# Kernel tuning notes

Measured on AMD Instinct MI355X. Metric: run time of the kernel, lower is better.

The kernel has to match this reference:

```python
import jax, jax.numpy as jnp
import numpy as np

N, NFEAT, NHID, NCLASS, E = 100000, 128, 128, 40, 1600000

def _glorot(key, fan_in, fan_out):
    lim = float(np.sqrt(6.0 / (fan_in + fan_out)))
    return jax.random.uniform(key, (fan_in, fan_out), jnp.float32, -lim, lim)

def setup_inputs() -> dict:
    key = jax.random.key(0)
    ks = jax.random.split(key, 20)
    inp = {
        'x': jax.random.normal(ks[0], (N, NFEAT), jnp.float32),
        'edge_index': jax.random.randint(ks[1], (2, E), 0, N, jnp.int64 if jax.config.x64_enabled else jnp.int32),
    }
    dims = [(NFEAT, NHID), (NHID, NHID), (NHID, NHID), (NHID, NHID), (NHID, NHID), (NHID, NHID)]
    names = ['gc1_w1', 'gc1_w2', 'gc2_w1', 'gc2_w2', 'gc3_w1', 'gc3_w2']
    for i, (nm, (fi, fo)) in enumerate(zip(names, dims)):
        inp[nm] = _glorot(ks[2 + i], fi, fo)
        inp[nm.replace('w', 'b')] = jnp.zeros((fo,), jnp.float32)
    inp['lin1_w'] = _glorot(ks[10], 3 * NHID, 3 * NHID)
    inp['lin1_b'] = jnp.zeros((3 * NHID,), jnp.float32)
    inp['lin2_w'] = _glorot(ks[11], 3 * NHID, NCLASS)
    inp['lin2_b'] = jnp.zeros((NCLASS,), jnp.float32)
    return inp

def _gin_conv(x, src, dst, w1, b1, w2, b2):
    # GINConv, eps=0: mlp(x + sum_{j->i} x_j)
    agg = jax.ops.segment_sum(x[src], dst, num_segments=N)  # [N, d]
    h = jax.nn.relu((x + agg) @ w1 + b1)
    return jax.nn.relu(h @ w2 + b2)

def reference(x, edge_index, gc1_w1, gc1_b1, gc1_w2, gc1_b2,
              gc2_w1, gc2_b1, gc2_w2, gc2_b2,
              gc3_w1, gc3_b1, gc3_w2, gc3_b2,
              lin1_w, lin1_b, lin2_w, lin2_b):
    src, dst = edge_index[0], edge_index[1]
    h1 = _gin_conv(x, src, dst, gc1_w1, gc1_b1, gc1_w2, gc1_b2)
    h2 = _gin_conv(h1, src, dst, gc2_w1, gc2_b1, gc2_w2, gc2_b2)
    h3 = _gin_conv(h2, src, dst, gc3_w1, gc3_b1, gc3_w2, gc3_b2)
    h = jnp.concatenate([h1, h2, h3], axis=1)  # [N, 3*nhid]
    h = jax.nn.relu(h @ lin1_w + lin1_b)  # dropout inactive in eval mode
    h = h @ lin2_w + lin2_b
    return jax.nn.log_softmax(h, axis=1)
```

## Files before the change

### kernel.cpp

```cpp
#include <hip/hip_runtime.h>

#define N_NODES 100000
#define NEDGE   1600000
#define NHID    128
#define NCLASS  40

#define AGG_NODES 128
#define COLV_LDS  3072
#define FILL_SLICES 8
#define FILL_RANGE  12500

using bf16x8 = __attribute__((ext_vector_type(8))) short;
using f32x4  = __attribute__((ext_vector_type(4))) float;

__device__ __forceinline__ float bf2f(unsigned short s) {
    unsigned u = ((unsigned)s) << 16; float f; __builtin_memcpy(&f, &u, 4); return f;
}
__device__ __forceinline__ unsigned short f2bf(float f) {
    unsigned u; __builtin_memcpy(&u, &f, 4);
    u = u + 0x7fffu + ((u >> 16) & 1u);
    return (unsigned short)(u >> 16);
}

__device__ __forceinline__ void gld16(const void* g, void* l) {
    __builtin_amdgcn_global_load_lds(g, l, 16, 0, 0);
}

__global__ void k_zero(int* __restrict__ p, int n) {
    int i = blockIdx.x * 256 + threadIdx.x;
    if (i < n) p[i] = 0;
}

__global__ void k_count(const int* __restrict__ ei, int* __restrict__ cnt) {
    int e = blockIdx.x * 256 + threadIdx.x;
    if (e < NEDGE) atomicAdd(&cnt[ei[NEDGE + e]], 1);
}

__global__ void k_scan1(const int* __restrict__ cnt, int* __restrict__ rp, int* __restrict__ bsum) {
    __shared__ int sh[256];
    int t = threadIdx.x, base = blockIdx.x * 1024;
    int v[4]; int s = 0;
    for (int k = 0; k < 4; ++k) { int i = base + t * 4 + k; v[k] = (i < N_NODES) ? cnt[i] : 0; s += v[k]; }
    sh[t] = s; __syncthreads();
    for (int off = 1; off < 256; off <<= 1) {
        int x = (t >= off) ? sh[t - off] : 0;
        __syncthreads();
        sh[t] += x;
        __syncthreads();
    }
    int excl = sh[t] - s;
    for (int k = 0; k < 4; ++k) { int i = base + t * 4 + k; if (i < N_NODES) rp[i] = excl; excl += v[k]; }
    if (t == 255) bsum[blockIdx.x] = sh[255];
}

__global__ void k_scan2(int* __restrict__ bsum, int nb) {
    __shared__ int sh[256];
    int t = threadIdx.x;
    int v = (t < nb) ? bsum[t] : 0;
    sh[t] = v; __syncthreads();
    for (int off = 1; off < 256; off <<= 1) {
        int x = (t >= off) ? sh[t - off] : 0;
        __syncthreads();
        sh[t] += x;
        __syncthreads();
    }
    if (t < nb) bsum[t] = sh[t] - v;
}

__global__ void k_scan3(int* __restrict__ rp, const int* __restrict__ bsum) {
    int base = blockIdx.x * 1024;
    int off = bsum[blockIdx.x];
    for (int k = 0; k < 4; ++k) {
        int i = base + threadIdx.x * 4 + k;
        if (i < N_NODES) rp[i] += off;
    }
    if (blockIdx.x == 0 && threadIdx.x == 0) rp[N_NODES] = NEDGE;
}

__global__ __launch_bounds__(256) void k_fillr(const int* __restrict__ ei, const int* __restrict__ rp,
                                               int* __restrict__ cur, int* __restrict__ colv) {
    int slice = blockIdx.x & 7;
    int e = (blockIdx.x >> 3) * 256 + threadIdx.x;
    if (e >= NEDGE) return;
    int d = ei[NEDGE + e];
    int lo = slice * FILL_RANGE;
    if (d >= lo && d < lo + FILL_RANGE) {
        int p = atomicAdd(&cur[d], 1);
        colv[rp[d] + p] = ei[e];
    }
}

__global__ void k_wprep(const float* __restrict__ w, unsigned short* __restrict__ wt,
                        int K, int O, int Opad) {
    int idx = blockIdx.x * 256 + threadIdx.x;
    if (idx >= K * Opad) return;
    int kss = K >> 5;
    int e = idx & 7, lane = (idx >> 3) & 63, rest = idx >> 9;
    int ks = rest % kss, ot = rest / kss;
    int c = ot * 16 + (lane & 15);
    int k = ks * 32 + (lane >> 4) * 8 + e;
    float v = (c < O) ? w[k * O + c] : 0.f;
    wt[idx] = f2bf(v);
}

__global__ void k_xprep(const float* __restrict__ x, unsigned short* __restrict__ xs) {
    int s = blockIdx.x & 7;
    int rest = (blockIdx.x >> 3) * 256 + threadIdx.x;
    if (rest >= N_NODES * 8) return;
    int n = rest >> 3, wrd = rest & 7;
    float2 v = *(const float2*)(x + (size_t)n * 128 + s * 16 + wrd * 2);
    ((unsigned*)xs)[(size_t)s * N_NODES * 8 + rest] =
        (unsigned)f2bf(v.x) | ((unsigned)f2bf(v.y) << 16);
}

__device__ __forceinline__ void acc8(float* acc, uint4 f, float m) {
    unsigned u[4] = {f.x, f.y, f.z, f.w};
    for (int d = 0; d < 4; ++d) {
        acc[2 * d]     = fmaf(m, bf2f((unsigned short)u[d]), acc[2 * d]);
        acc[2 * d + 1] = fmaf(m, bf2f((unsigned short)(u[d] >> 16)), acc[2 * d + 1]);
    }
}

__global__ __launch_bounds__(256) void k_aggs(const unsigned short* __restrict__ feat,
                                              unsigned short* __restrict__ tout,
                                              const int* __restrict__ rp,
                                              const int* __restrict__ colv) {
    __shared__ int scol[COLV_LDS];
    __shared__ int srp[AGG_NODES + 1];
    const int s = blockIdx.x & 7;
    const int chunk = blockIdx.x >> 3;
    const int tid = threadIdx.x;
    const int nbase = chunk * AGG_NODES;

    for (int i = tid; i <= AGG_NODES; i += 256) {
        int n = nbase + i;
        srp[i] = rp[n <= N_NODES ? n : N_NODES];
    }
    __syncthreads();
    const int ebase = srp[0];
    const int ecount = srp[AGG_NODES] - ebase;
    const int elds = ecount < COLV_LDS ? ecount : COLV_LDS;
    for (int i = tid; i < elds; i += 256) scol[i] = colv[ebase + i];
    __syncthreads();

    const unsigned* fs = (const unsigned*)feat + (size_t)s * N_NODES * 8;
    unsigned* ts = (unsigned*)tout + (size_t)s * N_NODES * 8;

    const int sub = tid >> 1, half = tid & 1;
    const int node = nbase + sub;
    if (node >= N_NODES) return;
    const int off = half * 4;
    const int e0 = srp[sub] - ebase, e1 = srp[sub + 1] - ebase;

    float acc[8];
    {
        uint4 a = *(const uint4*)(fs + (size_t)node * 8 + off);
        unsigned u[4] = {a.x, a.y, a.z, a.w};
        for (int d = 0; d < 4; ++d) {
            acc[2 * d]     = bf2f((unsigned short)u[d]);
            acc[2 * d + 1] = bf2f((unsigned short)(u[d] >> 16));
        }
    }

    for (int e = e0; e < e1; e += 8) {
        int j[8]; float m[8];
        #pragma unroll
        for (int k = 0; k < 8; ++k) {
            int ee = e + k;
            bool v = ee < e1;
            int idx = ee < COLV_LDS ? scol[ee] : colv[ebase + ee];
            j[k] = v ? idx : node;
            m[k] = v ? 1.f : 0.f;
        }
        uint4 f[8];
        #pragma unroll
        for (int k = 0; k < 8; ++k)
            f[k] = *(const uint4*)(fs + (size_t)j[k] * 8 + off);
        #pragma unroll
        for (int k = 0; k < 8; ++k) acc8(acc, f[k], m[k]);
    }

    uint4 o;
    o.x = (unsigned)f2bf(acc[0]) | ((unsigned)f2bf(acc[1]) << 16);
    o.y = (unsigned)f2bf(acc[2]) | ((unsigned)f2bf(acc[3]) << 16);
    o.z = (unsigned)f2bf(acc[4]) | ((unsigned)f2bf(acc[5]) << 16);
    o.w = (unsigned)f2bf(acc[6]) | ((unsigned)f2bf(acc[7]) << 16);
    *(uint4*)(ts + (size_t)node * 8 + off) = o;
}

__global__ __launch_bounds__(256) void k_mlp(
    const unsigned short* __restrict__ tin,
    const unsigned short* __restrict__ w1t, const float* __restrict__ b1,
    const unsigned short* __restrict__ w2t, const float* __restrict__ b2,
    unsigned short* __restrict__ hout) {
    __shared__ __align__(16) char tlds[64 * 256];
    __shared__ __align__(16) char hlds[64 * 256];
    const int tid = threadIdx.x, lane = tid & 63, w = tid >> 6;
    const int l15 = lane & 15, lg = lane >> 4;
    const int nbase = blockIdx.x * 64;

    #pragma unroll
    for (int i = 0; i < 4; ++i) {
        int byte = w * 4096 + i * 1024 + lane * 16;
        int r = byte >> 8, c8s = (byte >> 4) & 15;
        int c8 = c8s ^ (r & 7);
        int slice = c8 >> 1, half = c8 & 1;
        int node = nbase + r; if (node >= N_NODES) node = 0;
        gld16(tin + ((size_t)slice * N_NODES + node) * 16 + half * 8,
              tlds + w * 4096 + i * 1024);
    }

    bf16x8 B1[2][4]; float bias1[2]; int cols[2];
    #pragma unroll
    for (int ot = 0; ot < 2; ++ot) {
        int c = (w * 2 + ot) * 16 + l15;
        cols[ot] = c; bias1[ot] = b1[c];
        #pragma unroll
        for (int ks = 0; ks < 4; ++ks)
            B1[ot][ks] = *(const bf16x8*)(w1t + ((size_t)((w * 2 + ot) * 4 + ks) * 64 + lane) * 8);
    }
    __syncthreads();

    {
        bf16x8 A[2][4];
        #pragma unroll
        for (int ks = 0; ks < 4; ++ks)
            A[0][ks] = *(const bf16x8*)(tlds + l15 * 256 + ((ks * 64 + lg * 16) ^ ((l15 & 7) << 4)));
        #pragma unroll
        for (int m = 0; m < 4; ++m) {
            int cur = m & 1, nxt = cur ^ 1;
            if (m < 3) {
                int row = (m + 1) * 16 + l15;
                #pragma unroll
                for (int ks = 0; ks < 4; ++ks)
                    A[nxt][ks] = *(const bf16x8*)(tlds + row * 256 + ((ks * 64 + lg * 16) ^ ((row & 7) << 4)));
            }
            #pragma unroll
            for (int ot = 0; ot < 2; ++ot) {
                f32x4 acc = {0.f, 0.f, 0.f, 0.f};
                #pragma unroll
                for (int ks = 0; ks < 4; ++ks)
                    acc = __builtin_amdgcn_mfma_f32_16x16x32_bf16(A[cur][ks], B1[ot][ks], acc, 0, 0, 0);
                int c2 = cols[ot] * 2;
                #pragma unroll
                for (int r = 0; r < 4; ++r) {
                    int row = m * 16 + lg * 4 + r;
                    float v = acc[r] + bias1[ot]; v = v > 0.f ? v : 0.f;
                    *(unsigned short*)(hlds + row * 256 + (c2 ^ ((row & 7) << 4))) = f2bf(v);
                }
            }
        }
    }

    bf16x8 B2[2][4]; float bias2[2];
    #pragma unroll
    for (int ot = 0; ot < 2; ++ot) {
        bias2[ot] = b2[cols[ot]];
        #pragma unroll
        for (int ks = 0; ks < 4; ++ks)
            B2[ot][ks] = *(const bf16x8*)(w2t + ((size_t)((w * 2 + ot) * 4 + ks) * 64 + lane) * 8);
    }
    __syncthreads();

    {
        bf16x8 A[2][4];
        #pragma unroll
        for (int ks = 0; ks < 4; ++ks)
            A[0][ks] = *(const bf16x8*)(hlds + l15 * 256 + ((ks * 64 + lg * 16) ^ ((l15 & 7) << 4)));
        #pragma unroll
        for (int m = 0; m < 4; ++m) {
            int cur = m & 1, nxt = cur ^ 1;
            if (m < 3) {
                int row = (m + 1) * 16 + l15;
                #pragma unroll
                for (int ks = 0; ks < 4; ++ks)
                    A[nxt][ks] = *(const bf16x8*)(hlds + row * 256 + ((ks * 64 + lg * 16) ^ ((row & 7) << 4)));
            }
            #pragma unroll
            for (int ot = 0; ot < 2; ++ot) {
                f32x4 acc = {0.f, 0.f, 0.f, 0.f};
                #pragma unroll
                for (int ks = 0; ks < 4; ++ks)
                    acc = __builtin_amdgcn_mfma_f32_16x16x32_bf16(A[cur][ks], B2[ot][ks], acc, 0, 0, 0);
                int cslice = cols[ot] >> 4, cw = cols[ot] & 15;
                #pragma unroll
                for (int r = 0; r < 4; ++r) {
                    int node = nbase + m * 16 + lg * 4 + r;
                    if (node < N_NODES) {
                        float v = acc[r] + bias2[ot]; v = v > 0.f ? v : 0.f;
                        hout[((size_t)cslice * N_NODES + node) * 16 + cw] = f2bf(v);
                    }
                }
            }
        }
    }
}

__global__ __launch_bounds__(512, 2) void k_final(
    const unsigned short* __restrict__ h1, const unsigned short* __restrict__ h2,
    const unsigned short* __restrict__ h3,
    const unsigned short* __restrict__ l1t, const float* __restrict__ l1b,
    const unsigned short* __restrict__ l2t, const float* __restrict__ l2b,
    float* __restrict__ out) {
    extern __shared__ __align__(16) char lds[];
    const int tid = threadIdx.x, lane = tid & 63, w = tid >> 6;
    const int l15 = lane & 15, lg = lane >> 4;
    const int nbase = blockIdx.x * 128;

    #pragma unroll
    for (int i = 0; i < 12; ++i) {
        unsigned byte = (unsigned)(w * 12288 + i * 1024 + lane * 16);
        unsigned r = byte / 768u;
        unsigned rem = byte - r * 768u;
        int c8 = (int)(rem >> 4) ^ (int)(r & 7);
        int part = c8 >> 4, c8p = c8 & 15;
        int slice = c8p >> 1, half = c8p & 1;
        int node = nbase + (int)r; if (node >= N_NODES) node = 0;
        const unsigned short* hp = part == 0 ? h1 : (part == 1 ? h2 : h3);
        gld16(hp + ((size_t)slice * N_NODES + node) * 16 + half * 8,
              lds + w * 12288 + i * 1024);
    }

    bf16x8 B[2][3];
    #pragma unroll
    for (int ot = 0; ot < 3; ++ot)
        B[0][ot] = *(const bf16x8*)(l1t + ((size_t)((w * 3 + ot) * 12) * 64 + lane) * 8);
    __syncthreads();

    f32x4 acc[8][3];
    #pragma unroll
    for (int m = 0; m < 8; ++m)
        #pragma unroll
        for (int ot = 0; ot < 3; ++ot) acc[m][ot] = {0.f, 0.f, 0.f, 0.f};
    {
        #pragma unroll
        for (int ks = 0; ks < 12; ++ks) {
            int cur = ks & 1, nxt = cur ^ 1;
            if (ks < 11) {
                #pragma unroll
                for (int ot = 0; ot < 3; ++ot)
                    B[nxt][ot] = *(const bf16x8*)(l1t + ((size_t)((w * 3 + ot) * 12 + ks + 1) * 64 + lane) * 8);
            }
            bf16x8 A[8];
            #pragma unroll
            for (int m = 0; m < 8; ++m) {
                int row = m * 16 + l15;
                A[m] = *(const bf16x8*)(lds + row * 768 + ((ks * 64 + lg * 16) ^ ((row & 7) << 4)));
            }
            #pragma unroll
            for (int ot = 0; ot < 3; ++ot)
                #pragma unroll
                for (int m = 0; m < 8; ++m)
                    acc[m][ot] = __builtin_amdgcn_mfma_f32_16x16x32_bf16(A[m], B[cur][ot], acc[m][ot], 0, 0, 0);
        }
    }
    __syncthreads();

    #pragma unroll
    for (int ot = 0; ot < 3; ++ot) {
        int c = (w * 3 + ot) * 16 + l15;
        float bias = l1b[c];
        #pragma unroll
        for (int m = 0; m < 8; ++m)
            #pragma unroll
            for (int r = 0; r < 4; ++r) {
                int row = m * 16 + lg * 4 + r;
                float v = acc[m][ot][r] + bias; v = v > 0.f ? v : 0.f;
                *(unsigned short*)(lds + row * 768 + ((c * 2) ^ ((row & 7) << 4))) = f2bf(v);
            }
    }
    __syncthreads();

    f32x4 acc2[3];
    #pragma unroll
    for (int ot = 0; ot < 3; ++ot) acc2[ot] = {0.f, 0.f, 0.f, 0.f};
    {
        const int row = w * 16 + l15;
        bf16x8 C2[2][3]; bf16x8 A2[2];
        #pragma unroll
        for (int ot = 0; ot < 3; ++ot)
            C2[0][ot] = *(const bf16x8*)(l2t + ((size_t)(ot * 12) * 64 + lane) * 8);
        A2[0] = *(const bf16x8*)(lds + row * 768 + ((lg * 16) ^ ((row & 7) << 4)));
        #pragma unroll
        for (int ks = 0; ks < 12; ++ks) {
            int cur = ks & 1, nxt = cur ^ 1;
            if (ks < 11) {
                #pragma unroll
                for (int ot = 0; ot < 3; ++ot)
                    C2[nxt][ot] = *(const bf16x8*)(l2t + ((size_t)(ot * 12 + ks + 1) * 64 + lane) * 8);
                A2[nxt] = *(const bf16x8*)(lds + row * 768 + (((ks + 1) * 64 + lg * 16) ^ ((row & 7) << 4)));
            }
            #pragma unroll
            for (int ot = 0; ot < 3; ++ot)
                acc2[ot] = __builtin_amdgcn_mfma_f32_16x16x32_bf16(A2[cur], C2[cur][ot], acc2[ot], 0, 0, 0);
        }
    }

    int c0 = l15;
    #pragma unroll
    for (int r = 0; r < 4; ++r) {
        float v0 = acc2[0][r] + l2b[c0];
        float v1 = acc2[1][r] + l2b[c0 + 16];
        float v2 = (c0 < 8) ? (acc2[2][r] + l2b[c0 + 32]) : -1e30f;
        float mx = fmaxf(fmaxf(v0, v1), v2);
        for (int msk = 1; msk < 16; msk <<= 1) mx = fmaxf(mx, __shfl_xor(mx, msk));
        float s = __expf(v0 - mx) + __expf(v1 - mx) + ((c0 < 8) ? __expf(v2 - mx) : 0.f);
        for (int msk = 1; msk < 16; msk <<= 1) s += __shfl_xor(s, msk);
        float lse = mx + __logf(s);
        int node = nbase + w * 16 + lg * 4 + r;
        if (node < N_NODES) {
            out[(size_t)node * 40 + c0] = v0 - lse;
            out[(size_t)node * 40 + c0 + 16] = v1 - lse;
            if (c0 < 8) out[(size_t)node * 40 + c0 + 32] = v2 - lse;
        }
    }
}

extern "C" void kernel_launch(void* const* d_in, const int* in_sizes, int n_in,
                              void* d_out, int out_size, void* d_ws, size_t ws_size,
                              hipStream_t stream) {
    const float* x  = (const float*)d_in[0];
    const int*   ei = (const int*)d_in[1];
    const float* gw1[3] = {(const float*)d_in[2],  (const float*)d_in[6],  (const float*)d_in[10]};
    const float* gb1[3] = {(const float*)d_in[3],  (const float*)d_in[7],  (const float*)d_in[11]};
    const float* gw2[3] = {(const float*)d_in[4],  (const float*)d_in[8],  (const float*)d_in[12]};
    const float* gb2[3] = {(const float*)d_in[5],  (const float*)d_in[9],  (const float*)d_in[13]};
    const float* l1w = (const float*)d_in[14];
    const float* l1b = (const float*)d_in[15];
    const float* l2w = (const float*)d_in[16];
    const float* l2b = (const float*)d_in[17];
    float* out = (float*)d_out;

    char* p = (char*)d_ws;
    auto alloc = [&](size_t bytes) { char* q = p; p += (bytes + 255) & ~(size_t)255; return q; };
    int* rp   = (int*)alloc(4 * (N_NODES + 1));
    int* cnt  = (int*)alloc(4 * N_NODES);
    int* bsum = (int*)alloc(4 * 256);
    int* colv = (int*)alloc(4 * (size_t)NEDGE);
    unsigned short* t  = (unsigned short*)alloc(2 * (size_t)N_NODES * 128);
    unsigned short* h1 = (unsigned short*)alloc(2 * (size_t)N_NODES * 128);
    unsigned short* h2 = (unsigned short*)alloc(2 * (size_t)N_NODES * 128);
    unsigned short* h3 = (unsigned short*)alloc(2 * (size_t)N_NODES * 128);
    unsigned short* xs = h3;
    unsigned short* wt[6];
    for (int i = 0; i < 6; ++i) wt[i] = (unsigned short*)alloc(2 * 128 * 128);
    unsigned short* l1t = (unsigned short*)alloc(2 * 384 * 384);
    unsigned short* l2t = (unsigned short*)alloc(2 * 48 * 384);

    static bool attr_set = false;
    if (!attr_set) {
        hipFuncSetAttribute((const void*)k_final,
                            hipFuncAttributeMaxDynamicSharedMemorySize, 128 * 768);
        attr_set = true;
    }

    const int nb = (N_NODES + 1023) / 1024;
    k_zero<<<(N_NODES + 255) / 256, 256, 0, stream>>>(cnt, N_NODES);
    k_count<<<(NEDGE + 255) / 256, 256, 0, stream>>>(ei, cnt);
    k_scan1<<<nb, 256, 0, stream>>>(cnt, rp, bsum);
    k_scan2<<<1, 256, 0, stream>>>(bsum, nb);
    k_scan3<<<nb, 256, 0, stream>>>(rp, bsum);
    k_zero<<<(N_NODES + 255) / 256, 256, 0, stream>>>(cnt, N_NODES);
    k_fillr<<<((NEDGE + 255) / 256) * FILL_SLICES, 256, 0, stream>>>(ei, rp, cnt, colv);

    for (int i = 0; i < 3; ++i) {
        k_wprep<<<(128 * 128 + 255) / 256, 256, 0, stream>>>(gw1[i], wt[2 * i], 128, 128, 128);
        k_wprep<<<(128 * 128 + 255) / 256, 256, 0, stream>>>(gw2[i], wt[2 * i + 1], 128, 128, 128);
    }
    k_wprep<<<(384 * 384 + 255) / 256, 256, 0, stream>>>(l1w, l1t, 384, 384, 384);
    k_wprep<<<(384 * 48 + 255) / 256, 256, 0, stream>>>(l2w, l2t, 384, 40, 48);

    k_xprep<<<8 * ((N_NODES * 8 + 255) / 256), 256, 0, stream>>>(x, xs);

    const int gagg = ((N_NODES + AGG_NODES - 1) / AGG_NODES) * 8;
    const int gtile = (N_NODES + 63) / 64;
    const int gtile2 = (N_NODES + 127) / 128;
    k_aggs<<<gagg, 256, 0, stream>>>(xs, t, rp, colv);
    k_mlp<<<gtile, 256, 0, stream>>>(t, wt[0], gb1[0], wt[1], gb2[0], h1);
    k_aggs<<<gagg, 256, 0, stream>>>(h1, t, rp, colv);
    k_mlp<<<gtile, 256, 0, stream>>>(t, wt[2], gb1[1], wt[3], gb2[1], h2);
    k_aggs<<<gagg, 256, 0, stream>>>(h2, t, rp, colv);
    k_mlp<<<gtile, 256, 0, stream>>>(t, wt[4], gb1[2], wt[5], gb2[2], h3);
    k_final<<<gtile2, 512, 128 * 768, stream>>>(h1, h2, h3, l1t, l1b, l2t, l2b, out);
}
```

Measured before the change: 520.6 us.

## Merge weight-prep launches, slice edge counting, and deepen weight prefetch

The eight per-matrix weight conversion launches become one kernel that indexes across all weight matrices. That kernel writes into a single destination assumed to be contiguous with the later weight buffers, which relies on the allocator placing them back to back. Edge-degree counting now partitions destinations into eight ranges, as the fill kernel already does, to localize atomics, at the cost of re-reading the edge list eight times. The MLP kernel loads its second-layer weights before the first barrier, and the final kernel prefetches B fragments two steps ahead with a triple buffer, both to hide global-load latency at the cost of more registers.

```diff
diff --git a/kernel.cpp b/kernel.cpp
--- a/kernel.cpp
+++ b/kernel.cpp
@@ -9,6 +9,7 @@
 #define COLV_LDS  3072
 #define FILL_SLICES 8
 #define FILL_RANGE  12500
+#define WPREP_TOT   264192
 
 using bf16x8 = __attribute__((ext_vector_type(8))) short;
 using f32x4  = __attribute__((ext_vector_type(4))) float;
@@ -31,9 +32,13 @@
     if (i < n) p[i] = 0;
 }
 
-__global__ void k_count(const int* __restrict__ ei, int* __restrict__ cnt) {
-    int e = blockIdx.x * 256 + threadIdx.x;
-    if (e < NEDGE) atomicAdd(&cnt[ei[NEDGE + e]], 1);
+__global__ __launch_bounds__(256) void k_countr(const int* __restrict__ ei, int* __restrict__ cnt) {
+    int slice = blockIdx.x & 7;
+    int e = (blockIdx.x >> 3) * 256 + threadIdx.x;
+    if (e >= NEDGE) return;
+    int d = ei[NEDGE + e];
+    int lo = slice * FILL_RANGE;
+    if (d >= lo && d < lo + FILL_RANGE) atomicAdd(&cnt[d], 1);
 }
 
 __global__ void k_scan1(const int* __restrict__ cnt, int* __restrict__ rp, int* __restrict__ bsum) {
@@ -90,17 +95,29 @@
     }
 }
 
-__global__ void k_wprep(const float* __restrict__ w, unsigned short* __restrict__ wt,
-                        int K, int O, int Opad) {
+__global__ void k_wprep_all(const float* __restrict__ g0, const float* __restrict__ g1,
+                            const float* __restrict__ g2, const float* __restrict__ g3,
+                            const float* __restrict__ g4, const float* __restrict__ g5,
+                            const float* __restrict__ l1w, const float* __restrict__ l2w,
+                            unsigned short* __restrict__ dst) {
     int idx = blockIdx.x * 256 + threadIdx.x;
-    if (idx >= K * Opad) return;
+    if (idx >= WPREP_TOT) return;
+    const float* w; int local, K, O;
+    if (idx < 98304) {
+        int r = idx >> 14; local = idx & 16383; K = 128; O = 128;
+        w = r == 0 ? g0 : r == 1 ? g1 : r == 2 ? g2 : r == 3 ? g3 : r == 4 ? g4 : g5;
+    } else if (idx < 245760) {
+        local = idx - 98304; K = 384; O = 384; w = l1w;
+    } else {
+        local = idx - 245760; K = 384; O = 40; w = l2w;
+    }
     int kss = K >> 5;
-    int e = idx & 7, lane = (idx >> 3) & 63, rest = idx >> 9;
+    int e = local & 7, lane = (local >> 3) & 63, rest = local >> 9;
     int ks = rest % kss, ot = rest / kss;
     int c = ot * 16 + (lane & 15);
     int k = ks * 32 + (lane >> 4) * 8 + e;
     float v = (c < O) ? w[k * O + c] : 0.f;
-    wt[idx] = f2bf(v);
+    dst[idx] = f2bf(v);
 }
 
 __global__ void k_xprep(const float* __restrict__ x, unsigned short* __restrict__ xs) {
@@ -219,6 +236,14 @@
         for (int ks = 0; ks < 4; ++ks)
             B1[ot][ks] = *(const bf16x8*)(w1t + ((size_t)((w * 2 + ot) * 4 + ks) * 64 + lane) * 8);
     }
+    bf16x8 B2[2][4]; float bias2[2];
+    #pragma unroll
+    for (int ot = 0; ot < 2; ++ot) {
+        bias2[ot] = b2[(w * 2 + ot) * 16 + l15];
+        #pragma unroll
+        for (int ks = 0; ks < 4; ++ks)
+            B2[ot][ks] = *(const bf16x8*)(w2t + ((size_t)((w * 2 + ot) * 4 + ks) * 64 + lane) * 8);
+    }
     __syncthreads();
 
     {
@@ -250,15 +275,6 @@
                 }
             }
         }
-    }
-
-    bf16x8 B2[2][4]; float bias2[2];
-    #pragma unroll
-    for (int ot = 0; ot < 2; ++ot) {
-        bias2[ot] = b2[cols[ot]];
-        #pragma unroll
-        for (int ks = 0; ks < 4; ++ks)
-            B2[ot][ks] = *(const bf16x8*)(w2t + ((size_t)((w * 2 + ot) * 4 + ks) * 64 + lane) * 8);
     }
     __syncthreads();
 
@@ -321,10 +337,12 @@
               lds + w * 12288 + i * 1024);
     }
 
-    bf16x8 B[2][3];
-    #pragma unroll
-    for (int ot = 0; ot < 3; ++ot)
-        B[0][ot] = *(const bf16x8*)(l1t + ((size_t)((w * 3 + ot) * 12) * 64 + lane) * 8);
+    bf16x8 B[3][3];
+    #pragma unroll
+    for (int ot = 0; ot < 3; ++ot) {
+        B[0][ot] = *(const bf16x8*)(l1t + ((size_t)((w * 3 + ot) * 12 + 0) * 64 + lane) * 8);
+        B[1][ot] = *(const bf16x8*)(l1t + ((size_t)((w * 3 + ot) * 12 + 1) * 64 + lane) * 8);
+    }
     __syncthreads();
 
     f32x4 acc[8][3];
@@ -335,11 +353,12 @@
     {
         #pragma unroll
         for (int ks = 0; ks < 12; ++ks) {
-            int cur = ks & 1, nxt = cur ^ 1;
-            if (ks < 11) {
+            int cur = ks % 3;
+            if (ks < 10) {
+                int nx2 = (ks + 2) % 3;
                 #pragma unroll
                 for (int ot = 0; ot < 3; ++ot)
-                    B[nxt][ot] = *(const bf16x8*)(l1t + ((size_t)((w * 3 + ot) * 12 + ks + 1) * 64 + lane) * 8);
+                    B[nx2][ot] = *(const bf16x8*)(l1t + ((size_t)((w * 3 + ot) * 12 + ks + 2) * 64 + lane) * 8);
             }
             bf16x8 A[8];
             #pragma unroll
@@ -456,19 +475,15 @@
 
     const int nb = (N_NODES + 1023) / 1024;
     k_zero<<<(N_NODES + 255) / 256, 256, 0, stream>>>(cnt, N_NODES);
-    k_count<<<(NEDGE + 255) / 256, 256, 0, stream>>>(ei, cnt);
+    k_countr<<<((NEDGE + 255) / 256) * FILL_SLICES, 256, 0, stream>>>(ei, cnt);
     k_scan1<<<nb, 256, 0, stream>>>(cnt, rp, bsum);
     k_scan2<<<1, 256, 0, stream>>>(bsum, nb);
     k_scan3<<<nb, 256, 0, stream>>>(rp, bsum);
     k_zero<<<(N_NODES + 255) / 256, 256, 0, stream>>>(cnt, N_NODES);
     k_fillr<<<((NEDGE + 255) / 256) * FILL_SLICES, 256, 0, stream>>>(ei, rp, cnt, colv);
 
-    for (int i = 0; i < 3; ++i) {
-        k_wprep<<<(128 * 128 + 255) / 256, 256, 0, stream>>>(gw1[i], wt[2 * i], 128, 128, 128);
-        k_wprep<<<(128 * 128 + 255) / 256, 256, 0, stream>>>(gw2[i], wt[2 * i + 1], 128, 128, 128);
-    }
-    k_wprep<<<(384 * 384 + 255) / 256, 256, 0, stream>>>(l1w, l1t, 384, 384, 384);
-    k_wprep<<<(384 * 48 + 255) / 256, 256, 0, stream>>>(l2w, l2t, 384, 40, 48);
+    k_wprep_all<<<(WPREP_TOT + 255) / 256, 256, 0, stream>>>(
+        gw1[0], gw2[0], gw1[1], gw2[1], gw1[2], gw2[2], l1w, l2w, wt[0]);
 
     k_xprep<<<8 * ((N_NODES * 8 + 255) / 256), 256, 0, stream>>>(x, xs);
 
```

Measured after the change: 508.3 us. -2.4%, faster.
